# Kernel tuning notes

Hardware: AMD Instinct MI355X
Metric: run time of the kernel (lower is better)

Reference implementation:

```python
import jax, jax.numpy as jnp
import numpy as np

# ---- config (matches init_kwargs) ----
D_MODEL = 1024
D_STATE = 16
D_CONV = 4
EXPAND = 2
HEADDIM = 32
NGROUPS = 1
CHUNK = 256
D_INNER = EXPAND * D_MODEL            # 2048
NHEADS = D_INNER // HEADDIM           # 64
D_IN_PROJ = 2 * D_INNER + 2 * NGROUPS * D_STATE + NHEADS  # 4176
CONV_DIM = D_INNER + 2 * NGROUPS * D_STATE                # 2080
BATCH, SEQLEN = 2, 2048
EPS = 1e-5
NEG_INF = -1e9


def setup_inputs() -> dict:
    key = jax.random.key(0)
    ks = jax.random.split(key, 8)
    u = jax.random.normal(ks[0], (BATCH, SEQLEN, D_MODEL), jnp.float32)
    W_in = jax.random.normal(ks[1], (D_IN_PROJ, D_MODEL), jnp.float32) * (1.0 / np.sqrt(D_MODEL))
    conv_w = jax.random.normal(ks[2], (CONV_DIM, 1, D_CONV), jnp.float32) * (1.0 / np.sqrt(D_CONV))
    conv_b = jnp.zeros((CONV_DIM,), jnp.float32)
    dt_bias = jax.random.normal(ks[3], (NHEADS,), jnp.float32) * 0.1
    A_log = jnp.log(1.0 + 15.0 * jax.random.uniform(ks[4], (NHEADS,), jnp.float32))  # A in [1,16]
    D = jnp.ones((NHEADS,), jnp.float32)
    norm_w = jnp.ones((D_INNER,), jnp.float32)
    W_out = jax.random.normal(ks[5], (D_MODEL, D_INNER), jnp.float32) * (1.0 / np.sqrt(D_INNER))
    return dict(u=u, W_in=W_in, conv_w=conv_w, conv_b=conv_b, dt_bias=dt_bias,
                A_log=A_log, D=D, norm_w=norm_w, W_out=W_out)


def _ssd_chunk_scan(x, dt, A, Bm, Cm, Dh):
    """Mamba2 SSD chunked scan.
    x: (b,l,h,p), dt: (b,l,h), A: (h,), Bm/Cm: (b,l,n) [ngroups=1], Dh: (h,).
    """
    b, l, h, p = x.shape
    c = l // CHUNK
    n = Bm.shape[-1]
    xdt = x * dt[..., None]                                  # (b,l,h,p)
    xc = xdt.reshape(b, c, CHUNK, h, p)
    xo = x.reshape(b, c, CHUNK, h, p)
    Bc = Bm.reshape(b, c, CHUNK, n)
    Cc = Cm.reshape(b, c, CHUNK, n)
    Abar = (dt * A).reshape(b, c, CHUNK, h).transpose(0, 3, 1, 2)   # (b,h,c,l)
    Acum = jnp.cumsum(Abar, axis=-1)                                # (b,h,c,l)
    # intra-chunk decay matrix L[i,j] = exp(sum_{j<k<=i} Abar_k), causal
    seg = Acum[..., :, None] - Acum[..., None, :]                   # (b,h,c,l,l)
    causal = jnp.tril(jnp.ones((CHUNK, CHUNK), bool))
    Lmat = jnp.exp(jnp.where(causal, seg, NEG_INF))
    # diagonal (intra-chunk) contribution
    Yd = jnp.einsum('bcln,bcsn,bhcls,bcshp->bclhp', Cc, Bc, Lmat, xc)
    # chunk states
    decay_states = jnp.exp(Acum[..., -1:] - Acum)                   # (b,h,c,l)
    states = jnp.einsum('bcln,bhcl,bclhp->bchpn', Bc, decay_states, xc)
    chunk_decay = jnp.exp(Acum[..., -1])                            # (b,h,c)
    # inter-chunk recurrence over the c axis
    def step(carry, inp):
        s, dec = inp
        new = dec[..., None, None] * carry + s
        return new, carry
    s_t = jnp.moveaxis(states, 1, 0)            # (c,b,h,p,n)
    d_t = jnp.moveaxis(chunk_decay, -1, 0)      # (c,b,h)
    init = jnp.zeros((b, h, p, n), x.dtype)
    _, prev = jax.lax.scan(step, init, (s_t, d_t))
    prev = jnp.moveaxis(prev, 0, 1)             # (b,c,h,p,n) state entering each chunk
    Yo = jnp.einsum('bcln,bchpn,bhcl->bclhp', Cc, prev, jnp.exp(Acum))
    Y = Yd + Yo + xo * Dh[None, None, None, :, None]
    return Y.reshape(b, l, h, p)


def reference(u, W_in, conv_w, conv_b, dt_bias, A_log, D, norm_w, W_out):
    b, l, _ = u.shape
    zxbcdt = u @ W_in.T                                   # (b,l,D_IN_PROJ)
    z = zxbcdt[..., :D_INNER]
    xBC = zxbcdt[..., D_INNER:D_INNER + CONV_DIM]
    dt = jax.nn.softplus(zxbcdt[..., -NHEADS:] + dt_bias)  # (b,l,h)
    # depthwise causal conv1d + SiLU
    xBC_t = xBC.transpose(0, 2, 1)                        # (b, CONV_DIM, l)
    conv = jax.lax.conv_general_dilated(
        xBC_t, conv_w, window_strides=(1,), padding=[(D_CONV - 1, 0)],
        feature_group_count=CONV_DIM)
    xBC = jax.nn.silu(conv + conv_b[None, :, None]).transpose(0, 2, 1)
    x = xBC[..., :D_INNER]
    Bm = xBC[..., D_INNER:D_INNER + NGROUPS * D_STATE]
    Cm = xBC[..., D_INNER + NGROUPS * D_STATE:]
    A = -jnp.exp(A_log)
    Y = _ssd_chunk_scan(x.reshape(b, l, NHEADS, HEADDIM), dt, A, Bm, Cm, D)
    y = Y.reshape(b, l, D_INNER)
    # gated RMSNorm (norm_before_gate=False): normalize(y * silu(z)) * w
    yg = y * jax.nn.silu(z)
    yn = yg * jax.lax.rsqrt(jnp.mean(yg * yg, axis=-1, keepdims=True) + EPS) * norm_w
    out = yn @ W_out.T
    return (out, z)
```

## Files before the change

### kernel.cpp

```cpp
#include <hip/hip_runtime.h>

#define BATCH   2
#define SEQLEN  2048
#define DMODEL  1024
#define DINNER  2048
#define NHEADS  64
#define HEADDIM 32
#define DSTATE  16
#define CONVDIM 2080
#define DINPROJ 4192
#define NPAD    4352
#define CHUNK   256
#define NCHUNK  8
#define BL      (BATCH*SEQLEN)
#define XWIDTH  2144

typedef float          f4    __attribute__((ext_vector_type(4)));
typedef short          s16x8 __attribute__((ext_vector_type(8)));
typedef unsigned short u16x4 __attribute__((ext_vector_type(4)));
typedef __bf16         bf16x8 __attribute__((ext_vector_type(8)));
typedef float          f32x4v __attribute__((ext_vector_type(4)));

#define MFMA16(a,b,c) __builtin_amdgcn_mfma_f32_16x16x32_bf16((a),(b),(c),0,0,0)

__device__ __forceinline__ unsigned short f2bf(float f){
  unsigned int u = __float_as_uint(f);
  u += 0x7FFFu + ((u >> 16) & 1u);
  return (unsigned short)(u >> 16);
}
__device__ __forceinline__ float bf2f(unsigned short u){
  return __uint_as_float(((unsigned int)u) << 16);
}

__device__ __forceinline__ void gload_lds16(const void* g, void* l){
  __builtin_amdgcn_global_load_lds((const __attribute__((address_space(1))) unsigned int*)g,
                                   (__attribute__((address_space(3))) unsigned int*)l,
                                   16, 0, 0);
}

__device__ __forceinline__ bf16x8 f32x8_to_frag(const float* src, bool valid){
  bf16x8 r;
  if (valid) {
    f4 a = *(const f4*)src;
    f4 c = *(const f4*)(src + 4);
    r[0]=(__bf16)a[0]; r[1]=(__bf16)a[1]; r[2]=(__bf16)a[2]; r[3]=(__bf16)a[3];
    r[4]=(__bf16)c[0]; r[5]=(__bf16)c[1]; r[6]=(__bf16)c[2]; r[7]=(__bf16)c[3];
  } else {
    r[0]=(__bf16)0.f; r[1]=(__bf16)0.f; r[2]=(__bf16)0.f; r[3]=(__bf16)0.f;
    r[4]=(__bf16)0.f; r[5]=(__bf16)0.f; r[6]=(__bf16)0.f; r[7]=(__bf16)0.f;
  }
  return r;
}

__device__ __forceinline__ bf16x8 bf16x8_load(const unsigned short* src, bool valid){
  if (valid) {
    s16x8 v = *(const s16x8*)src;
    return *(bf16x8*)&v;
  }
  bf16x8 r;
  r[0]=(__bf16)0.f; r[1]=(__bf16)0.f; r[2]=(__bf16)0.f; r[3]=(__bf16)0.f;
  r[4]=(__bf16)0.f; r[5]=(__bf16)0.f; r[6]=(__bf16)0.f; r[7]=(__bf16)0.f;
  return r;
}

__global__ void cast_f32_bf16(const float* __restrict__ in, unsigned short* __restrict__ out, int n){
  int i = blockIdx.x * 256 + threadIdx.x;
  if (i < n) out[i] = f2bf(in[i]);
}

__global__ void cast_win_pad(const float* __restrict__ in, unsigned short* __restrict__ out){
  int i = blockIdx.x * 256 + threadIdx.x;
  if (i >= NPAD * DMODEL) return;
  int r = i >> 10;
  out[i] = (r < DINPROJ) ? f2bf(in[i]) : (unsigned short)0;
}

__global__ __launch_bounds__(512) void gemm256_in(
    const unsigned short* __restrict__ A,
    const unsigned short* __restrict__ B,
    float* __restrict__ C0, float* __restrict__ C1)
{
  __shared__ unsigned short As[2][2][128][64];
  __shared__ unsigned short Bs[2][2][128][64];
  const int K = DMODEL;

  const int nx   = gridDim.x;
  const int flat = blockIdx.y * nx + blockIdx.x;
  const int q    = (nx * gridDim.y) >> 3;
  const int swz  = (flat & 7) * q + (flat >> 3);
  const int bm   = swz / nx, bn = swz % nx;

  const int tid  = threadIdx.x;
  const int wave = tid >> 6, lane = tid & 63;
  const int wr   = wave >> 2, wc = wave & 3;
  const int l16  = lane & 15, khalf = lane >> 4;

  const int srow8  = lane >> 3;
  const int schunk = (lane & 7) ^ srow8;
  const unsigned short* Asrc = A + (size_t)(bm * 256 + wave * 8 + srow8) * K + schunk * 8;
  const unsigned short* Bsrc = B + (size_t)(bn * 256 + wave * 8 + srow8) * K + schunk * 8;

  auto stageHalf = [&](int buf, int kind, int k0){
    const unsigned short* s = (kind < 2) ? (Asrc + (size_t)(kind & 1) * 128 * K + k0)
                                         : (Bsrc + (size_t)(kind & 1) * 128 * K + k0);
    unsigned short* d = (kind < 2) ? &As[buf][kind & 1][wave * 8][0]
                                   : &Bs[buf][kind & 1][wave * 8][0];
    gload_lds16(s, d);
    gload_lds16(s + (size_t)64 * K, d + 4096);
  };

#define AFRAG(i,ks) (*(const bf16x8*)&As[cur][wr][(i)*16 + l16][((((ks)*4 + khalf)) ^ (l16 & 7)) * 8])
#define BFRAG(n,ks) (*(const bf16x8*)&Bs[cur][wc >> 1][(wc & 1)*64 + (n)*16 + l16][((((ks)*4 + khalf)) ^ (l16 & 7)) * 8])

  f32x4v acc[8][4];
  #pragma unroll
  for (int i = 0; i < 8; ++i)
    #pragma unroll
    for (int j = 0; j < 4; ++j)
      acc[i][j] = (f32x4v){0.f,0.f,0.f,0.f};

  stageHalf(0, 0, 0); stageHalf(0, 1, 0); stageHalf(0, 2, 0); stageHalf(0, 3, 0);
  asm volatile("s_waitcnt vmcnt(0)" ::: "memory");
  __builtin_amdgcn_s_barrier();
  __builtin_amdgcn_sched_barrier(0);

  const int NT = K >> 6;
  for (int t = 0; t < NT; ++t) {
    const int cur = t & 1, nxt = cur ^ 1;
    const int k1 = (t + 1) << 6;
    bf16x8 bfm[4][2];
    #pragma unroll
    for (int p = 0; p < 4; ++p) {
      bf16x8 a00 = AFRAG(2*p,   0), a01 = AFRAG(2*p,   1);
      bf16x8 a10 = AFRAG(2*p+1, 0), a11 = AFRAG(2*p+1, 1);
      if (p == 0) {
        #pragma unroll
        for (int n = 0; n < 4; ++n) { bfm[n][0] = BFRAG(n,0); bfm[n][1] = BFRAG(n,1); }
      }
      if (t + 1 < NT) stageHalf(nxt, p, k1);
      asm volatile("s_waitcnt lgkmcnt(0)" ::: "memory");
      __builtin_amdgcn_sched_barrier(0);
      __builtin_amdgcn_s_barrier();
      __builtin_amdgcn_sched_barrier(0);
      __builtin_amdgcn_s_setprio(1);
      #pragma unroll
      for (int n = 0; n < 4; ++n) {
        acc[2*p][n]   = MFMA16(a00, bfm[n][0], acc[2*p][n]);
        acc[2*p][n]   = MFMA16(a01, bfm[n][1], acc[2*p][n]);
        acc[2*p+1][n] = MFMA16(a10, bfm[n][0], acc[2*p+1][n]);
        acc[2*p+1][n] = MFMA16(a11, bfm[n][1], acc[2*p+1][n]);
      }
      __builtin_amdgcn_s_setprio(0);
      __builtin_amdgcn_sched_barrier(0);
    }
    if (t + 1 < NT) {
      asm volatile("s_waitcnt vmcnt(0)" ::: "memory");
      __builtin_amdgcn_s_barrier();
      __builtin_amdgcn_sched_barrier(0);
    }
  }
#undef AFRAG
#undef BFRAG

  const int orow0 = bm * 256 + wr * 128;
  const int ocol0 = bn * 256 + wc * 64;
  #pragma unroll
  for (int mi = 0; mi < 8; ++mi)
    #pragma unroll
    for (int ni = 0; ni < 4; ++ni) {
      int col  = ocol0 + ni * 16 + l16;
      int rowb = orow0 + mi * 16 + khalf * 4;
      #pragma unroll
      for (int r = 0; r < 4; ++r) {
        float v = acc[mi][ni][r];
        int row = rowb + r;
        if (col < DINNER)        C0[(size_t)row * DINNER + col] = v;
        else if (col < DINPROJ)  C1[(size_t)row * XWIDTH + (col - DINNER)] = v;
      }
    }
}

__global__ __launch_bounds__(256) void gemm_bf16_out(
    const unsigned short* __restrict__ A,
    const unsigned short* __restrict__ B,
    int K, float* __restrict__ C0, int N)
{
  __shared__ unsigned short As[2][128][32];
  __shared__ unsigned short Bs[2][128][32];

  const int nx   = gridDim.x;
  const int flat = blockIdx.y * nx + blockIdx.x;
  const int q    = (nx * gridDim.y) >> 3;
  const int swz  = (flat & 7) * q + (flat >> 3);
  const int bm   = swz / nx, bn = swz % nx;

  const int tid  = threadIdx.x;
  const int wave = tid >> 6, lane = tid & 63;
  const int wm   = (wave >> 1) * 64, wn = (wave & 1) * 64;
  const int lrow = lane & 15, khalf = lane >> 4;
  const int cread = (khalf ^ ((lrow >> 1) & 3)) * 8;

  const int srow = wave * 16 + (lane >> 2);
  const int scol = ((lane & 3) ^ ((lane >> 3) & 3)) * 8;
  const unsigned short* Ag = A + (size_t)(bm * 128 + srow) * K + scol;
  const unsigned short* Bg = B + (size_t)(bn * 128 + srow) * K + scol;
  const int lr0 = wave * 16;

  f32x4v acc[4][4];
  #pragma unroll
  for (int i = 0; i < 4; ++i)
    #pragma unroll
    for (int j = 0; j < 4; ++j)
      acc[i][j] = (f32x4v){0.f,0.f,0.f,0.f};

  auto stage = [&](int buf, int k0){
    gload_lds16(Ag + k0,                   &As[buf][lr0][0]);
    gload_lds16(Ag + k0 + (size_t)64 * K,  &As[buf][64 + lr0][0]);
    gload_lds16(Bg + k0,                   &Bs[buf][lr0][0]);
    gload_lds16(Bg + k0 + (size_t)64 * K,  &Bs[buf][64 + lr0][0]);
  };

  const int NT = K >> 5;
  stage(0, 0);
  stage(1, 32);
  for (int t = 0; t < NT; ++t) {
    const int cur = t & 1;
    if (t + 1 < NT) { asm volatile("s_waitcnt vmcnt(4)" ::: "memory"); }
    else            { asm volatile("s_waitcnt vmcnt(0)" ::: "memory"); }
    __builtin_amdgcn_s_barrier();
    __builtin_amdgcn_sched_barrier(0);
    bf16x8 af[4], bfr[4];
    #pragma unroll
    for (int i = 0; i < 4; ++i) {
      af[i]  = *(const bf16x8*)&As[cur][wm + i * 16 + lrow][cread];
      bfr[i] = *(const bf16x8*)&Bs[cur][wn + i * 16 + lrow][cread];
    }
    __builtin_amdgcn_s_setprio(1);
    #pragma unroll
    for (int mi = 0; mi < 4; ++mi)
      #pragma unroll
      for (int ni = 0; ni < 4; ++ni)
        acc[mi][ni] = MFMA16(af[mi], bfr[ni], acc[mi][ni]);
    __builtin_amdgcn_s_setprio(0);
    __builtin_amdgcn_s_barrier();
    __builtin_amdgcn_sched_barrier(0);
    if (t + 2 < NT) stage(cur, (t + 2) << 5);
  }

  const int orow0 = bm * 128 + wm;
  const int ocol0 = bn * 128 + wn;
  #pragma unroll
  for (int mi = 0; mi < 4; ++mi)
    #pragma unroll
    for (int ni = 0; ni < 4; ++ni) {
      int col  = ocol0 + ni * 16 + lrow;
      int rowb = orow0 + mi * 16 + khalf * 4;
      #pragma unroll
      for (int r = 0; r < 4; ++r)
        C0[(size_t)(rowb + r) * N + col] = acc[mi][ni][r];
    }
}

__global__ void conv_dt_kernel(const float* __restrict__ xbcdt,
                               const float* __restrict__ conv_w, const float* __restrict__ conv_b,
                               const float* __restrict__ dt_bias,
                               unsigned short* __restrict__ xconv, float* __restrict__ dtout)
{
  int idx = blockIdx.x * 256 + threadIdx.x;
  if (idx >= BL * XWIDTH) return;
  int ch = idx % XWIDTH;
  int bl = idx / XWIDTH;
  int l  = bl & (SEQLEN - 1);
  if (ch < CONVDIM) {
    float acc = conv_b[ch];
    #pragma unroll
    for (int j = 0; j < 4; ++j) {
      int ls = l - 3 + j;
      float x = (ls >= 0) ? xbcdt[(size_t)(bl - 3 + j) * XWIDTH + ch] : 0.f;
      acc += conv_w[ch * 4 + j] * x;
    }
    float s = acc / (1.f + __expf(-acc));
    xconv[(size_t)bl * CONVDIM + ch] = f2bf(s);
  } else {
    int h = ch - CONVDIM;
    float x = xbcdt[(size_t)bl * XWIDTH + ch] + dt_bias[h];
    float dtv = (x > 20.f) ? x : log1pf(__expf(x));
    dtout[bl * NHEADS + h] = dtv;
  }
}

__global__ __launch_bounds__(256) void ssd_phaseA(
    const unsigned short* __restrict__ xconv, const float* __restrict__ dt,
    const float* __restrict__ A_log,
    float* __restrict__ acum, float* __restrict__ decay, float* __restrict__ states)
{
  int bc = blockIdx.x, h = blockIdx.y;
  int b = bc >> 3;
  int t = threadIdx.x;
  __shared__ float sAc[256], sCoef[256], sDt[256];
  __shared__ float sB[256][16];
  __shared__ float sX[256][32];
  int rowbase = b * SEQLEN + (bc & 7) * CHUNK;
  float dtv = dt[(rowbase + t) * NHEADS + h];
  float Av  = -__expf(A_log[h]);
  sAc[t] = dtv * Av; sDt[t] = dtv;
  for (int i = t; i < 256 * 16; i += 256) { int l = i >> 4, n = i & 15; sB[l][n] = bf2f(xconv[(size_t)(rowbase + l) * CONVDIM + DINNER + n]); }
  for (int i = t; i < 256 * 32; i += 256) { int l = i >> 5, p = i & 31; sX[l][p] = bf2f(xconv[(size_t)(rowbase + l) * CONVDIM + h * 32 + p]); }
  __syncthreads();
  for (int off = 1; off < 256; off <<= 1) {
    float add = (t >= off) ? sAc[t - off] : 0.f;
    __syncthreads();
    sAc[t] += add;
    __syncthreads();
  }
  int bch = bc * 64 + h;
  acum[(size_t)bch * 256 + t] = sAc[t];
  float last = sAc[255];
  if (t == 0) decay[bch] = __expf(last);
  sCoef[t] = sDt[t] * __expf(last - sAc[t]);
  __syncthreads();
  #pragma unroll
  for (int o = 0; o < 2; ++o) {
    int oi = t + o * 256;
    int p = oi >> 4, n = oi & 15;
    float acc = 0.f;
    for (int l = 0; l < 256; ++l) acc += sCoef[l] * sB[l][n] * sX[l][p];
    states[(size_t)bch * 512 + oi] = acc;
  }
}

__global__ void ssd_phaseB(const float* __restrict__ states, const float* __restrict__ decay,
                           float* __restrict__ prev)
{
  int bh = blockIdx.x;
  int b = bh >> 6, h = bh & 63;
  int t = threadIdx.x;
  float carry = 0.f;
  for (int c = 0; c < NCHUNK; ++c) {
    int bch = (b * 8 + c) * 64 + h;
    size_t base = (size_t)bch * 512 + t;
    prev[base] = carry;
    carry = decay[bch] * carry + states[base];
  }
}

__global__ __launch_bounds__(256, 2) void ssd_phaseC_mfma(
    const unsigned short* __restrict__ xconv, const float* __restrict__ dt,
    const float* __restrict__ acum, const float* __restrict__ prev,
    const float* __restrict__ Dvec, float* __restrict__ y)
{
  const int bc = blockIdx.x, h = blockIdx.y;
  const int b = bc >> 3;
  const int rowbase = b * SEQLEN + (bc & 7) * CHUNK;
  const int bch = bc * 64 + h;
  const int tid = threadIdx.x, wave = tid >> 6, lane = tid & 63;
  const int l16 = lane & 15, khalf = lane >> 4;

  __shared__ float sAcum[256];
  __shared__ __bf16 sXT[32][264];
  __shared__ __bf16 sP[4][2][16][40];

  if (tid < 256) sAcum[tid] = acum[(size_t)bch * 256 + tid];
  {
    int l  = tid >> 3;
    int p0 = (tid & 7) * 4;
    #pragma unroll
    for (int pass = 0; pass < 8; ++pass) {
      int ls = l + pass * 32;
      const unsigned short* xr = xconv + (size_t)(rowbase + ls) * CONVDIM + h * 32 + p0;
      u16x4 v = *(const u16x4*)xr;
      float dtl = dt[(rowbase + ls) * NHEADS + h];
      #pragma unroll
      for (int j = 0; j < 4; ++j) sXT[p0 + j][ls] = (__bf16)(bf2f(v[j]) * dtl);
    }
  }

  const bool kv = (khalf < 2);
  bf16x8 bfr[16], cfr[4], pvf[2];
  #pragma unroll
  for (int i = 0; i < 16; ++i)
    bfr[i] = bf16x8_load(xconv + (size_t)(rowbase + i * 16 + l16) * CONVDIM + DINNER + khalf * 8, kv);
  #pragma unroll
  for (int t = 0; t < 4; ++t)
    cfr[t] = bf16x8_load(xconv + (size_t)(rowbase + (wave + 4 * t) * 16 + l16) * CONVDIM + DINNER + DSTATE + khalf * 8, kv);
  #pragma unroll
  for (int pt = 0; pt < 2; ++pt)
    pvf[pt] = f32x8_to_frag(prev + (size_t)bch * 512 + (pt * 16 + l16) * 16 + khalf * 8, kv);
  __syncthreads();

  const float Dh = Dvec[h];
  #pragma unroll
  for (int t = 0; t < 4; ++t) {
    const int LT = wave + 4 * t;
    const int lbase = LT * 16;
    float al[4], el[4];
    #pragma unroll
    for (int r = 0; r < 4; ++r) { al[r] = sAcum[lbase + khalf * 4 + r]; el[r] = __expf(al[r]); }
    f32x4v y0 = MFMA16(cfr[t], pvf[0], ((f32x4v){0.f,0.f,0.f,0.f}));
    f32x4v y1 = MFMA16(cfr[t], pvf[1], ((f32x4v){0.f,0.f,0.f,0.f}));
    #pragma unroll
    for (int r = 0; r < 4; ++r) { y0[r] *= el[r]; y1[r] *= el[r]; }

    #pragma unroll
    for (int kp = 0; kp < 8; ++kp) {
      if (2 * kp <= LT) {
        f32x4v s0 = MFMA16(cfr[t], bfr[2 * kp],     ((f32x4v){0.f,0.f,0.f,0.f}));
        f32x4v s1 = MFMA16(cfr[t], bfr[2 * kp + 1], ((f32x4v){0.f,0.f,0.f,0.f}));
        const int buf = kp & 1;
        #pragma unroll
        for (int r = 0; r < 4; ++r) {
          int l  = lbase + khalf * 4 + r;
          int sA = 2 * kp * 16 + l16;
          int sB2 = sA + 16;
          float p0 = (sA  <= l) ? s0[r] * __expf(al[r] - sAcum[sA])  : 0.f;
          float p1 = (sB2 <= l) ? s1[r] * __expf(al[r] - sAcum[sB2]) : 0.f;
          sP[wave][buf][khalf * 4 + r][l16]      = (__bf16)p0;
          sP[wave][buf][khalf * 4 + r][16 + l16] = (__bf16)p1;
        }
        bf16x8 pa  = *(const bf16x8*)&sP[wave][buf][l16][khalf * 8];
        bf16x8 xf0 = *(const bf16x8*)&sXT[l16][kp * 32 + khalf * 8];
        bf16x8 xf1 = *(const bf16x8*)&sXT[16 + l16][kp * 32 + khalf * 8];
        y0 = MFMA16(pa, xf0, y0);
        y1 = MFMA16(pa, xf1, y1);
      }
    }

    #pragma unroll
    for (int r = 0; r < 4; ++r) {
      int lg = rowbase + lbase + khalf * 4 + r;
      const unsigned short* xr = xconv + (size_t)lg * CONVDIM + h * 32;
      float* yr = y + (size_t)lg * DINNER + h * 32;
      yr[l16]      = y0[r] + Dh * bf2f(xr[l16]);
      yr[16 + l16] = y1[r] + Dh * bf2f(xr[16 + l16]);
    }
  }
}

__global__ __launch_bounds__(256) void gate_norm(const float* __restrict__ y,
    const float* __restrict__ z, const float* __restrict__ norm_w,
    unsigned short* __restrict__ ynbf)
{
  int row = blockIdx.x, t = threadIdx.x;
  const float* yr = y + (size_t)row * DINNER;
  const float* zr = z + (size_t)row * DINNER;
  float vals[8];
  float ss = 0.f;
  #pragma unroll
  for (int i = 0; i < 8; ++i) {
    int ci = t + i * 256;
    float zv = zr[ci];
    float g = zv / (1.f + __expf(-zv));
    float v = yr[ci] * g;
    vals[i] = v; ss += v * v;
  }
  #pragma unroll
  for (int o = 1; o < 64; o <<= 1) ss += __shfl_xor(ss, o);
  __shared__ float sred[4];
  if ((t & 63) == 0) sred[t >> 6] = ss;
  __syncthreads();
  float tot = sred[0] + sred[1] + sred[2] + sred[3];
  float scale = rsqrtf(tot * (1.f / DINNER) + 1e-5f);
  #pragma unroll
  for (int i = 0; i < 8; ++i) {
    int ci = t + i * 256;
    ynbf[(size_t)row * DINNER + ci] = f2bf(vals[i] * scale * norm_w[ci]);
  }
}

extern "C" void kernel_launch(void* const* d_in, const int* in_sizes, int n_in,
                              void* d_out, int out_size, void* d_ws, size_t ws_size,
                              hipStream_t stream)
{
  const float* u       = (const float*)d_in[0];
  const float* W_in    = (const float*)d_in[1];
  const float* conv_w  = (const float*)d_in[2];
  const float* conv_b  = (const float*)d_in[3];
  const float* dt_bias = (const float*)d_in[4];
  const float* A_log   = (const float*)d_in[5];
  const float* Dv      = (const float*)d_in[6];
  const float* norm_w  = (const float*)d_in[7];
  const float* W_out   = (const float*)d_in[8];

  float* out  = (float*)d_out;
  float* zout = out + (size_t)BL * DMODEL;

  char* ws = (char*)d_ws;
  size_t off = 0;
  auto alloc = [&](size_t bytes){ size_t o = off; off += (bytes + 255) & ~(size_t)255; return o; };
  size_t o_ubf    = alloc((size_t)BL * DMODEL * 2);
  size_t o_wbf    = alloc((size_t)NPAD * DMODEL * 2);
  size_t o_xbcdt  = alloc((size_t)BL * XWIDTH * 4);
  size_t o_xconv  = alloc((size_t)BL * CONVDIM * 2);
  size_t o_dt     = alloc((size_t)BL * NHEADS * 4);
  size_t o_acum   = alloc((size_t)1024 * 256 * 4);
  size_t o_decay  = alloc((size_t)1024 * 4);
  size_t o_states = alloc((size_t)1024 * 512 * 4);
  size_t o_prev   = alloc((size_t)1024 * 512 * 4);
  size_t o_ynbf   = alloc((size_t)BL * DINNER * 2);

  unsigned short* ubf    = (unsigned short*)(ws + o_ubf);
  unsigned short* wbf    = (unsigned short*)(ws + o_wbf);
  float*          xbcdt  = (float*)(ws + o_xbcdt);
  unsigned short* xconv  = (unsigned short*)(ws + o_xconv);
  float*          dtws   = (float*)(ws + o_dt);
  float*          acum   = (float*)(ws + o_acum);
  float*          decay  = (float*)(ws + o_decay);
  float*          states = (float*)(ws + o_states);
  float*          prevb  = (float*)(ws + o_prev);
  unsigned short* ynbf   = (unsigned short*)(ws + o_ynbf);
  unsigned short* woutbf = ubf;
  float*          ywork  = xbcdt;

  cast_f32_bf16<<<(BL * DMODEL) / 256, 256, 0, stream>>>(u, ubf, BL * DMODEL);
  cast_win_pad<<<(NPAD * DMODEL) / 256, 256, 0, stream>>>(W_in, wbf);

  gemm256_in<<<dim3(NPAD / 256, BL / 256), 512, 0, stream>>>(ubf, wbf, zout, xbcdt);

  conv_dt_kernel<<<(BL * XWIDTH) / 256, 256, 0, stream>>>(xbcdt, conv_w, conv_b, dt_bias, xconv, dtws);

  ssd_phaseA<<<dim3(16, 64), 256, 0, stream>>>(xconv, dtws, A_log, acum, decay, states);
  ssd_phaseB<<<128, 512, 0, stream>>>(states, decay, prevb);
  ssd_phaseC_mfma<<<dim3(16, 64), 256, 0, stream>>>(xconv, dtws, acum, prevb, Dv, ywork);

  gate_norm<<<BL, 256, 0, stream>>>(ywork, zout, norm_w, ynbf);

  cast_f32_bf16<<<(DMODEL * DINNER) / 256, 256, 0, stream>>>(W_out, woutbf, DMODEL * DINNER);

  gemm_bf16_out<<<dim3(DMODEL / 128, BL / 128), 256, 0, stream>>>(ynbf, woutbf, DINNER, out, DMODEL);
}
```

Before: 233.0 us.

## Restructure input GEMM pipeline and store xBC as bf16 with separate dt buffer

The input-projection GEMM switches from a per-quarter staged double buffer with four barriers per k-step to a two-deep prefetch: both buffers are loaded up front and each iteration waits on partial vmcnt, then refills the buffer it just consumed. The GEMM epilogue now writes the xBC columns as bf16 and the dt columns to a separate fp32 buffer. The conv kernel reads these narrower buffers. This reduces synchronisation in the main loop and the bytes written and reread between the GEMM and conv kernels. The tradeoffs are extra bf16 rounding of the pre-conv activations and a dedicated y workspace that can no longer alias the xBC buffer.

```diff
diff --git a/kernel.cpp b/kernel.cpp
--- a/kernel.cpp
+++ b/kernel.cpp
@@ -78,10 +78,11 @@
 __global__ __launch_bounds__(512) void gemm256_in(
     const unsigned short* __restrict__ A,
     const unsigned short* __restrict__ B,
-    float* __restrict__ C0, float* __restrict__ C1)
-{
-  __shared__ unsigned short As[2][2][128][64];
-  __shared__ unsigned short Bs[2][2][128][64];
+    float* __restrict__ Cz, unsigned short* __restrict__ Cx,
+    float* __restrict__ dtraw)
+{
+  __shared__ unsigned short As[2][256][64];
+  __shared__ unsigned short Bs[2][256][64];
   const int K = DMODEL;
 
   const int nx   = gridDim.x;
@@ -96,21 +97,20 @@
   const int l16  = lane & 15, khalf = lane >> 4;
 
   const int srow8  = lane >> 3;
-  const int schunk = (lane & 7) ^ srow8;
-  const unsigned short* Asrc = A + (size_t)(bm * 256 + wave * 8 + srow8) * K + schunk * 8;
-  const unsigned short* Bsrc = B + (size_t)(bn * 256 + wave * 8 + srow8) * K + schunk * 8;
-
-  auto stageHalf = [&](int buf, int kind, int k0){
-    const unsigned short* s = (kind < 2) ? (Asrc + (size_t)(kind & 1) * 128 * K + k0)
-                                         : (Bsrc + (size_t)(kind & 1) * 128 * K + k0);
-    unsigned short* d = (kind < 2) ? &As[buf][kind & 1][wave * 8][0]
-                                   : &Bs[buf][kind & 1][wave * 8][0];
-    gload_lds16(s, d);
-    gload_lds16(s + (size_t)64 * K, d + 4096);
+  const int scol   = ((lane & 7) ^ srow8) * 8;
+  const unsigned short* Asrc = A + (size_t)(bm * 256 + wave * 8 + srow8) * K + scol;
+  const unsigned short* Bsrc = B + (size_t)(bn * 256 + wave * 8 + srow8) * K + scol;
+
+  auto stage = [&](int buf, int k0){
+    #pragma unroll
+    for (int j = 0; j < 4; ++j) {
+      gload_lds16(Asrc + (size_t)j * 64 * K + k0, &As[buf][j * 64 + wave * 8][0]);
+      gload_lds16(Bsrc + (size_t)j * 64 * K + k0, &Bs[buf][j * 64 + wave * 8][0]);
+    }
   };
 
-#define AFRAG(i,ks) (*(const bf16x8*)&As[cur][wr][(i)*16 + l16][((((ks)*4 + khalf)) ^ (l16 & 7)) * 8])
-#define BFRAG(n,ks) (*(const bf16x8*)&Bs[cur][wc >> 1][(wc & 1)*64 + (n)*16 + l16][((((ks)*4 + khalf)) ^ (l16 & 7)) * 8])
+#define AFR(i,ks) (*(const bf16x8*)&As[cur][wr * 128 + (i) * 16 + l16][((((ks) * 4 + khalf) ^ (l16 & 7))) * 8])
+#define BFR(n,ks) (*(const bf16x8*)&Bs[cur][wc * 64 + (n) * 16 + l16][((((ks) * 4 + khalf) ^ (l16 & 7))) * 8])
 
   f32x4v acc[8][4];
   #pragma unroll
@@ -119,48 +119,35 @@
     for (int j = 0; j < 4; ++j)
       acc[i][j] = (f32x4v){0.f,0.f,0.f,0.f};
 
-  stageHalf(0, 0, 0); stageHalf(0, 1, 0); stageHalf(0, 2, 0); stageHalf(0, 3, 0);
-  asm volatile("s_waitcnt vmcnt(0)" ::: "memory");
-  __builtin_amdgcn_s_barrier();
-  __builtin_amdgcn_sched_barrier(0);
-
   const int NT = K >> 6;
+  stage(0, 0);
+  stage(1, 64);
   for (int t = 0; t < NT; ++t) {
-    const int cur = t & 1, nxt = cur ^ 1;
-    const int k1 = (t + 1) << 6;
+    const int cur = t & 1;
+    if (t + 1 < NT) { asm volatile("s_waitcnt vmcnt(8)" ::: "memory"); }
+    else            { asm volatile("s_waitcnt vmcnt(0)" ::: "memory"); }
+    __builtin_amdgcn_s_barrier();
+    __builtin_amdgcn_sched_barrier(0);
     bf16x8 bfm[4][2];
     #pragma unroll
-    for (int p = 0; p < 4; ++p) {
-      bf16x8 a00 = AFRAG(2*p,   0), a01 = AFRAG(2*p,   1);
-      bf16x8 a10 = AFRAG(2*p+1, 0), a11 = AFRAG(2*p+1, 1);
-      if (p == 0) {
-        #pragma unroll
-        for (int n = 0; n < 4; ++n) { bfm[n][0] = BFRAG(n,0); bfm[n][1] = BFRAG(n,1); }
-      }
-      if (t + 1 < NT) stageHalf(nxt, p, k1);
-      asm volatile("s_waitcnt lgkmcnt(0)" ::: "memory");
-      __builtin_amdgcn_sched_barrier(0);
-      __builtin_amdgcn_s_barrier();
-      __builtin_amdgcn_sched_barrier(0);
-      __builtin_amdgcn_s_setprio(1);
+    for (int n = 0; n < 4; ++n) { bfm[n][0] = BFR(n,0); bfm[n][1] = BFR(n,1); }
+    __builtin_amdgcn_s_setprio(1);
+    #pragma unroll
+    for (int mi = 0; mi < 8; ++mi) {
+      bf16x8 a0 = AFR(mi,0), a1 = AFR(mi,1);
       #pragma unroll
       for (int n = 0; n < 4; ++n) {
-        acc[2*p][n]   = MFMA16(a00, bfm[n][0], acc[2*p][n]);
-        acc[2*p][n]   = MFMA16(a01, bfm[n][1], acc[2*p][n]);
-        acc[2*p+1][n] = MFMA16(a10, bfm[n][0], acc[2*p+1][n]);
-        acc[2*p+1][n] = MFMA16(a11, bfm[n][1], acc[2*p+1][n]);
+        acc[mi][n] = MFMA16(a0, bfm[n][0], acc[mi][n]);
+        acc[mi][n] = MFMA16(a1, bfm[n][1], acc[mi][n]);
       }
-      __builtin_amdgcn_s_setprio(0);
-      __builtin_amdgcn_sched_barrier(0);
-    }
-    if (t + 1 < NT) {
-      asm volatile("s_waitcnt vmcnt(0)" ::: "memory");
-      __builtin_amdgcn_s_barrier();
-      __builtin_amdgcn_sched_barrier(0);
-    }
-  }
-#undef AFRAG
-#undef BFRAG
+    }
+    __builtin_amdgcn_s_setprio(0);
+    __builtin_amdgcn_s_barrier();
+    __builtin_amdgcn_sched_barrier(0);
+    if (t + 2 < NT) stage(cur, (t + 2) << 6);
+  }
+#undef AFR
+#undef BFR
 
   const int orow0 = bm * 256 + wr * 128;
   const int ocol0 = bn * 256 + wc * 64;
@@ -174,8 +161,13 @@
       for (int r = 0; r < 4; ++r) {
         float v = acc[mi][ni][r];
         int row = rowb + r;
-        if (col < DINNER)        C0[(size_t)row * DINNER + col] = v;
-        else if (col < DINPROJ)  C1[(size_t)row * XWIDTH + (col - DINNER)] = v;
+        if (col < DINNER) {
+          Cz[(size_t)row * DINNER + col] = v;
+        } else if (col < DINPROJ) {
+          int xcol = col - DINNER;
+          Cx[(size_t)row * XWIDTH + xcol] = f2bf(v);
+          if (xcol >= CONVDIM) dtraw[(size_t)row * NHEADS + (xcol - CONVDIM)] = v;
+        }
       }
     }
 }
@@ -261,7 +253,8 @@
     }
 }
 
-__global__ void conv_dt_kernel(const float* __restrict__ xbcdt,
+__global__ void conv_dt_kernel(const unsigned short* __restrict__ xbc,
+                               const float* __restrict__ dtraw,
                                const float* __restrict__ conv_w, const float* __restrict__ conv_b,
                                const float* __restrict__ dt_bias,
                                unsigned short* __restrict__ xconv, float* __restrict__ dtout)
@@ -276,14 +269,14 @@
     #pragma unroll
     for (int j = 0; j < 4; ++j) {
       int ls = l - 3 + j;
-      float x = (ls >= 0) ? xbcdt[(size_t)(bl - 3 + j) * XWIDTH + ch] : 0.f;
+      float x = (ls >= 0) ? bf2f(xbc[(size_t)(bl - 3 + j) * XWIDTH + ch]) : 0.f;
       acc += conv_w[ch * 4 + j] * x;
     }
     float s = acc / (1.f + __expf(-acc));
     xconv[(size_t)bl * CONVDIM + ch] = f2bf(s);
   } else {
     int h = ch - CONVDIM;
-    float x = xbcdt[(size_t)bl * XWIDTH + ch] + dt_bias[h];
+    float x = dtraw[(size_t)bl * NHEADS + h] + dt_bias[h];
     float dtv = (x > 20.f) ? x : log1pf(__expf(x));
     dtout[bl * NHEADS + h] = dtv;
   }
@@ -489,34 +482,37 @@
   auto alloc = [&](size_t bytes){ size_t o = off; off += (bytes + 255) & ~(size_t)255; return o; };
   size_t o_ubf    = alloc((size_t)BL * DMODEL * 2);
   size_t o_wbf    = alloc((size_t)NPAD * DMODEL * 2);
-  size_t o_xbcdt  = alloc((size_t)BL * XWIDTH * 4);
+  size_t o_xbc    = alloc((size_t)BL * XWIDTH * 2);
+  size_t o_dtraw  = alloc((size_t)BL * NHEADS * 4);
   size_t o_xconv  = alloc((size_t)BL * CONVDIM * 2);
   size_t o_dt     = alloc((size_t)BL * NHEADS * 4);
   size_t o_acum   = alloc((size_t)1024 * 256 * 4);
   size_t o_decay  = alloc((size_t)1024 * 4);
   size_t o_states = alloc((size_t)1024 * 512 * 4);
   size_t o_prev   = alloc((size_t)1024 * 512 * 4);
+  size_t o_ywork  = alloc((size_t)BL * DINNER * 4);
   size_t o_ynbf   = alloc((size_t)BL * DINNER * 2);
 
   unsigned short* ubf    = (unsigned short*)(ws + o_ubf);
   unsigned short* wbf    = (unsigned short*)(ws + o_wbf);
-  float*          xbcdt  = (float*)(ws + o_xbcdt);
+  unsigned short* xbc    = (unsigned short*)(ws + o_xbc);
+  float*          dtraw  = (float*)(ws + o_dtraw);
   unsigned short* xconv  = (unsigned short*)(ws + o_xconv);
   float*          dtws   = (float*)(ws + o_dt);
   float*          acum   = (float*)(ws + o_acum);
   float*          decay  = (float*)(ws + o_decay);
   float*          states = (float*)(ws + o_states);
   float*          prevb  = (float*)(ws + o_prev);
+  float*          ywork  = (float*)(ws + o_ywork);
   unsigned short* ynbf   = (unsigned short*)(ws + o_ynbf);
   unsigned short* woutbf = ubf;
-  float*          ywork  = xbcdt;
 
   cast_f32_bf16<<<(BL * DMODEL) / 256, 256, 0, stream>>>(u, ubf, BL * DMODEL);
   cast_win_pad<<<(NPAD * DMODEL) / 256, 256, 0, stream>>>(W_in, wbf);
 
-  gemm256_in<<<dim3(NPAD / 256, BL / 256), 512, 0, stream>>>(ubf, wbf, zout, xbcdt);
-
-  conv_dt_kernel<<<(BL * XWIDTH) / 256, 256, 0, stream>>>(xbcdt, conv_w, conv_b, dt_bias, xconv, dtws);
+  gemm256_in<<<dim3(NPAD / 256, BL / 256), 512, 0, stream>>>(ubf, wbf, zout, xbc, dtraw);
+
+  conv_dt_kernel<<<(BL * XWIDTH) / 256, 256, 0, stream>>>(xbc, dtraw, conv_w, conv_b, dt_bias, xconv, dtws);
 
   ssd_phaseA<<<dim3(16, 64), 256, 0, stream>>>(xconv, dtws, A_log, acum, decay, states);
   ssd_phaseB<<<128, 512, 0, stream>>>(states, decay, prevb);
```

Measured after the change: 249.3 us. +7.0%, slower.
